# Kernel optimization log

Measured on AMD Instinct MI355X. Metric: run time of the kernel, lower is better.

## Reference

```python
import jax, jax.numpy as jnp
import numpy as np
from jax import lax


def _gru_pass(x_proj, h0, w_hh, b_hh):
    # Faithful to torch: unbatched GRU scanning sequentially over the n_sample axis
    # with a single shared hidden state. x_proj: (N, 3H) = x @ w_ih.T + b_ih.
    def cell(h, xp):
        gh = jnp.dot(w_hh, h) + b_hh              # (3H,)
        xr, xz, xn = jnp.split(xp, 3)
        hr, hz, hn = jnp.split(gh, 3)
        r = jax.nn.sigmoid(xr + hr)
        z = jax.nn.sigmoid(xz + hz)
        n = jnp.tanh(xn + r * hn)
        h_new = (1.0 - z) * n + z * h
        return h_new, h_new
    h_last, outs = lax.scan(cell, h0, x_proj)
    return outs, h_last                            # (N, H), (H,)


def setup_inputs() -> dict:
    key = jax.random.key(0)
    ks = jax.random.split(key, 6)
    H = 50
    s = 0.2  # ~ torch default init scale for these fan-ins
    return {
        "w_ih": jax.random.normal(ks[0], (3 * H, 2), jnp.float32) * s,
        "w_hh": jax.random.normal(ks[1], (3 * H, H), jnp.float32) * s,
        "b_ih": jax.random.normal(ks[2], (3 * H,), jnp.float32) * s,
        "b_hh": jax.random.normal(ks[3], (3 * H,), jnp.float32) * s,
        "fc_w": jax.random.normal(ks[4], (2, H), jnp.float32) * s,
        "fc_b": jax.random.normal(ks[5], (2,), jnp.float32) * s,
        "sorb": 64,
        "n_sample": 4096,
    }


def reference(w_ih, w_hh, b_ih, b_hh, fc_w, fc_b, sorb, n_sample):
    H = w_hh.shape[1]
    baseline = float(sorb // 2 - 1)
    base_key = jax.random.key(42)
    x0 = jnp.zeros((n_sample, 2), jnp.float32)     # samples[:, 0, :] == 0
    h0 = jnp.zeros((H,), jnp.float32)
    nup0 = jnp.zeros((n_sample,), jnp.float32)

    def heaviside(x):
        # 0.5*(sign(sign(x)+0.1)+1): 1 for x >= 0, else 0
        return (x >= 0.0).astype(jnp.float32)

    def step(carry, i):
        x, h, num_up = carry
        x_proj = x @ w_ih.T + b_ih                 # (N, 3H)
        outs, h_new = _gru_pass(x_proj, h, w_hh, b_hh)
        logits = outs @ fc_w.T + fc_b              # (N, 2)
        out = jnp.sqrt(jax.nn.softmax(logits, axis=1))  # sqsoftmax
        # occupation-number masking, active for i >= sorb/2
        num_down = i.astype(jnp.float32) - num_up
        act_up = heaviside(baseline - num_up)
        act_down = heaviside(baseline - num_down)
        masked = out * jnp.stack([act_down, act_up], axis=1)
        masked = masked / jnp.clip(
            jnp.linalg.norm(masked, axis=1, keepdims=True), 1e-30, None)
        out = jnp.where(i >= sorb / 2, masked, out)
        # multinomial over 2 classes (weights need not sum to 1)
        p0 = out[:, 0] / jnp.clip(out[:, 0] + out[:, 1], 1e-30, None)
        u = jax.random.uniform(jax.random.fold_in(base_key, i), (n_sample,))
        s = (u >= p0).astype(jnp.int32)            # 1 == class 1 ("up")
        x_next = jax.nn.one_hot(s, 2, dtype=jnp.float32)
        return (x_next, h_new, num_up + s.astype(jnp.float32)), s

    _, samples = lax.scan(step, (x0, h0, nup0), jnp.arange(sorb))
    # torch returns argmax over the one-hot == sampled class index
    return samples.T                                # (n_sample, sorb) int32
```

## Files before the change

### kernel.cpp

```cpp
#include <hip/hip_runtime.h>
#include <cstdint>

#pragma clang fp contract(off)

#define HH 50
#define SORB 64
#define NSAMP 4096
#define TOT (SORB * NSAMP)
#define RSLOTS 128
#define RSTRIDE 56
#define SPIN_FUEL (1 << 16)

typedef __attribute__((ext_vector_type(2))) float v2f;
typedef __attribute__((ext_vector_type(4))) float v4f;

__device__ __forceinline__ float xla_tanh(float x) {
  const float kClamp = 7.90531110763549805f;
  float ax = fabsf(x);
  float xc = fminf(fmaxf(x, -kClamp), kClamp);
  float x2 = xc * xc;
  float p = -2.76076847742355e-16f;
  p = x2 * p + 2.00018790482477e-13f;
  p = x2 * p + -8.60467152213735e-11f;
  p = x2 * p + 5.12229709037114e-08f;
  p = x2 * p + 1.48572235717979e-05f;
  p = x2 * p + 6.37261928875436e-04f;
  p = x2 * p + 4.89352455891786e-03f;
  p = xc * p;
  float q = 1.19825839466702e-06f;
  q = x2 * q + 1.18534705686654e-04f;
  q = x2 * q + 2.26843463243900e-03f;
  q = x2 * q + 4.89352518554385e-03f;
  float r = p / q;
  return (ax < 0.0004f) ? x : r;
}

__device__ __forceinline__ float xla_logistic(float x) {
  return 0.5f + 0.5f * xla_tanh(x * 0.5f);
}

__device__ __forceinline__ float exp_cr(float x) {
  return (float)exp((double)x);
}

__device__ __forceinline__ void tf2x32(uint32_t k0, uint32_t k1,
                                       uint32_t c0, uint32_t c1,
                                       uint32_t& o0, uint32_t& o1) {
  uint32_t k2 = k0 ^ k1 ^ 0x1BD11BDAu;
  uint32_t x0 = c0 + k0, x1 = c1 + k1;
#define TF_R(d) { x0 += x1; x1 = (x1 << (d)) | (x1 >> (32 - (d))); x1 ^= x0; }
#define TF_GA TF_R(13) TF_R(15) TF_R(26) TF_R(6)
#define TF_GB TF_R(17) TF_R(29) TF_R(16) TF_R(24)
  TF_GA; x0 += k1; x1 += k2 + 1u;
  TF_GB; x0 += k2; x1 += k0 + 2u;
  TF_GA; x0 += k0; x1 += k1 + 3u;
  TF_GB; x0 += k1; x1 += k2 + 4u;
  TF_GA; x0 += k2; x1 += k0 + 5u;
#undef TF_GB
#undef TF_GA
#undef TF_R
  o0 = x0; o1 = x1;
}

__device__ __forceinline__ float u_for_cell(int cc) {
  int ii = cc >> 12;
  int jj = cc & (NSAMP - 1);
  uint32_t k0, k1;
  tf2x32(0u, 42u, 0u, (uint32_t)ii, k0, k1);
  uint32_t b0, b1;
  tf2x32(k0, k1, 0u, (uint32_t)jj, b0, b1);
  uint32_t bits = b0 ^ b1;
  return __uint_as_float((bits >> 9) | 0x3f800000u) - 1.0f;
}

__device__ __forceinline__ float dot_xla(const v2f* __restrict__ w,
                                         const v2f* __restrict__ h) {
  v2f A0 = w[0] * h[0];
  v2f A1 = w[1] * h[1];
  v2f A2 = w[2] * h[2];
  v2f A3 = w[3] * h[3];
#pragma unroll
  for (int ch = 1; ch < 6; ++ch) {
    A0 = A0 + w[4 * ch + 0] * h[4 * ch + 0];
    A1 = A1 + w[4 * ch + 1] * h[4 * ch + 1];
    A2 = A2 + w[4 * ch + 2] * h[4 * ch + 2];
    A3 = A3 + w[4 * ch + 3] * h[4 * ch + 3];
  }
  v2f S0 = A0 + A2;
  v2f S1 = A1 + A3;
  v2f T = S0 + S1;
  float dot = T.x + T.y;
  dot = dot + w[24].x * h[24].x;
  dot = dot + w[24].y * h[24].y;
  return dot;
}

extern "C" __global__ void __launch_bounds__(128, 1)
ARSampler_59244778881183_kernel(const float* __restrict__ w_ih,
                                const float* __restrict__ w_hh,
                                const float* __restrict__ b_ih,
                                const float* __restrict__ b_hh,
                                const float* __restrict__ fc_w,
                                const float* __restrict__ fc_b,
                                int* __restrict__ out) {
  __shared__ __align__(16) float ring[RSLOTS][RSTRIDE];
  __shared__ float sh_nu[NSAMP];
  __shared__ unsigned char sh_bits[2][NSAMP];
  __shared__ unsigned int sh_done;

  const int t = threadIdx.x;
  const int lane = t & 63;

  if (t < 64) {
    for (int s = lane; s < RSLOTS; s += 64)
      ring[s][HH] = __uint_as_float(~0u);
    if (lane < HH) ring[RSLOTS - 1][lane] = 0.0f;
  } else {
    if (lane == 0) sh_done = 0u;
    for (int q = lane; q < NSAMP; q += 64) sh_nu[q] = 0.0f;
  }
  __syncthreads();

  if (t < 64) {
    const int tr = (lane < HH) ? lane : 0;

    v2f wA[25], wB[25], wC[25];
#pragma unroll
    for (int k = 0; k < 25; ++k) {
      wA[k] = v2f{w_hh[tr * HH + 2 * k], w_hh[tr * HH + 2 * k + 1]};
      wB[k] = v2f{w_hh[(tr + 50) * HH + 2 * k], w_hh[(tr + 50) * HH + 2 * k + 1]};
      wC[k] = v2f{w_hh[(tr + 100) * HH + 2 * k], w_hh[(tr + 100) * HH + 2 * k + 1]};
    }
    const float bhr = b_hh[tr], bhz = b_hh[tr + 50], bhn = b_hh[tr + 100];
    const float xrb = b_ih[tr], xzb = b_ih[tr + 50], xnb = b_ih[tr + 100];
    const float xr0 = w_ih[tr * 2 + 0] + xrb;
    const float xr1 = w_ih[tr * 2 + 1] + xrb;
    const float xz0 = w_ih[(tr + 50) * 2 + 0] + xzb;
    const float xz1 = w_ih[(tr + 50) * 2 + 1] + xzb;
    const float xn0 = w_ih[(tr + 100) * 2 + 0] + xnb;
    const float xn1 = w_ih[(tr + 100) * 2 + 1] + xnb;
    float hold = 0.0f;

    volatile unsigned int* donep = &sh_done;

    for (int c = 0; c < TOT; ++c) {
      const int i = c >> 12;
      const int j = c & (NSAMP - 1);

      if ((c & 63) == 0 && c >= RSLOTS) {
        int fuel = SPIN_FUEL;
        while (*donep < (unsigned)(c - 64) && --fuel)
          __builtin_amdgcn_s_sleep(2);
        asm volatile("" ::: "memory");
      }

      const float* rp = ring[(c + RSLOTS - 1) & (RSLOTS - 1)];
      v2f hv[25];
#pragma unroll
      for (int m = 0; m < 13; ++m) {
        v4f f = *(const v4f*)(rp + 4 * m);
        hv[2 * m] = v2f{f.x, f.y};
        if (2 * m + 1 < 25) hv[2 * m + 1] = v2f{f.z, f.w};
      }

      float xr, xz, xn;
      if (i == 0) {
        xr = xrb; xz = xzb; xn = xnb;
      } else {
        unsigned b = sh_bits[(i - 1) & 1][j];
        xr = b ? xr1 : xr0;
        xz = b ? xz1 : xz0;
        xn = b ? xn1 : xn0;
      }

      const float ghr = dot_xla(wA, hv) + bhr;
      const float ghz = dot_xla(wB, hv) + bhz;
      const float ghn = dot_xla(wC, hv) + bhn;

      const float r = xla_logistic(xr + ghr);
      const float z = xla_logistic(xz + ghz);
      const float rhn = r * ghn;
      const float n = xla_tanh(xn + rhn);
      const float omz = 1.0f - z;
      const float hnew = omz * n + z * hold;
      hold = hnew;

      const int wi = (lane < HH) ? lane : HH;
      const float wd = (lane < HH) ? hnew : __uint_as_float((unsigned)c);
      ring[c & (RSLOTS - 1)][wi] = wd;
    }
  } else {
    float fw0[HH], fw1[HH];
#pragma unroll
    for (int k = 0; k < HH; ++k) {
      fw0[k] = fc_w[k];
      fw1[k] = fc_w[HH + k];
    }
    const float fb0 = fc_b[0], fb1 = fc_b[1];

    for (int B = 0; B < TOT; B += 64) {
      const int cc = B + lane;
      const int ii = B >> 12;
      const int jj = cc & (NSAMP - 1);

      {
        const unsigned target = (unsigned)(B + 63);
        volatile unsigned int* sp =
            (volatile unsigned int*)&ring[(B + 63) & (RSLOTS - 1)][HH];
        int fuel = SPIN_FUEL;
        while (*sp != target && --fuel) __builtin_amdgcn_s_sleep(2);
        __builtin_amdgcn_s_sleep(1);
        asm volatile("s_waitcnt lgkmcnt(0)" ::: "memory");
      }

      const float* op = ring[cc & (RSLOTS - 1)];
      float o[52];
#pragma unroll
      for (int m = 0; m < 13; ++m) {
        v4f f = *(const v4f*)(op + 4 * m);
        o[4 * m + 0] = f.x; o[4 * m + 1] = f.y;
        o[4 * m + 2] = f.z; o[4 * m + 3] = f.w;
      }

      float l0 = 0.0f, l1 = 0.0f;
#pragma unroll
      for (int k = 0; k < HH; ++k) {
        l0 = fmaf(o[k], fw0[k], l0);
        l1 = fmaf(o[k], fw1[k], l1);
      }
      l0 = l0 + fb0;
      l1 = l1 + fb1;

      const float mx = fmaxf(l0, l1);
      const float e0 = exp_cr(l0 - mx);
      const float e1 = exp_cr(l1 - mx);
      const float se = e0 + e1;
      float o0 = sqrtf(e0 / se);
      float o1 = sqrtf(e1 / se);

      const float nuo = sh_nu[jj];
      if (ii >= SORB / 2) {
        const float fi = (float)ii;
        const float ndown = fi - nuo;
        const float ad = ((31.0f - ndown) >= 0.0f) ? 1.0f : 0.0f;
        const float au = ((31.0f - nuo) >= 0.0f) ? 1.0f : 0.0f;
        const float m0 = o0 * ad;
        const float m1 = o1 * au;
        float nr = sqrtf(m0 * m0 + m1 * m1);
        nr = fmaxf(nr, 1e-30f);
        o0 = m0 / nr;
        o1 = m1 / nr;
      }
      const float den = fmaxf(o0 + o1, 1e-30f);
      const float p0 = o0 / den;
      const float u = u_for_cell(cc);
      const int s = (u >= p0) ? 1 : 0;

      sh_nu[jj] = nuo + (float)s;
      sh_bits[ii & 1][jj] = (unsigned char)s;
      out[jj * SORB + ii] = s;

      asm volatile("" ::: "memory");
      *(volatile unsigned int*)&sh_done = (unsigned)(B + 64);
    }
  }
}

extern "C" void kernel_launch(void* const* d_in, const int* in_sizes, int n_in,
                              void* d_out, int out_size, void* d_ws, size_t ws_size,
                              hipStream_t stream) {
  (void)in_sizes; (void)n_in; (void)out_size; (void)d_ws; (void)ws_size;
  const float* w_ih = (const float*)d_in[0];
  const float* w_hh = (const float*)d_in[1];
  const float* b_ih = (const float*)d_in[2];
  const float* b_hh = (const float*)d_in[3];
  const float* fc_w = (const float*)d_in[4];
  const float* fc_b = (const float*)d_in[5];
  hipLaunchKernelGGL(ARSampler_59244778881183_kernel, dim3(1), dim3(128), 0, stream,
                     w_ih, w_hh, b_ih, b_hh, fc_w, fc_b, (int*)d_out);
}
```

Measured before the change: 169.6 ms.

## Split GRU gate matvecs across three wavefronts with LDS flag handoff

New measurement: 196.7 ms. 1.16x slower.

```diff
diff --git a/kernel.cpp b/kernel.cpp
--- a/kernel.cpp
+++ b/kernel.cpp
@@ -95,7 +95,14 @@
   return dot;
 }
 
-extern "C" __global__ void __launch_bounds__(128, 1)
+#define SPIN_EQ(addr, target) do {                                           \
+  volatile unsigned int* sp_ = (volatile unsigned int*)(addr);               \
+  int fuel_ = SPIN_FUEL;                                                     \
+  while (*sp_ != (unsigned)(target) && --fuel_) {}                           \
+  asm volatile("s_waitcnt lgkmcnt(0)" ::: "memory");                         \
+} while (0)
+
+extern "C" __global__ void __launch_bounds__(256, 1)
 ARSampler_59244778881183_kernel(const float* __restrict__ w_ih,
                                 const float* __restrict__ w_hh,
                                 const float* __restrict__ b_ih,
@@ -104,41 +111,40 @@
                                 const float* __restrict__ fc_b,
                                 int* __restrict__ out) {
   __shared__ __align__(16) float ring[RSLOTS][RSTRIDE];
+  __shared__ float ghr[RSTRIDE];
+  __shared__ float ghz[RSTRIDE];
   __shared__ float sh_nu[NSAMP];
   __shared__ unsigned char sh_bits[2][NSAMP];
   __shared__ unsigned int sh_done;
 
   const int t = threadIdx.x;
   const int lane = t & 63;
-
-  if (t < 64) {
+  const int wv = t >> 6;
+
+  if (wv == 0) {
     for (int s = lane; s < RSLOTS; s += 64)
       ring[s][HH] = __uint_as_float(~0u);
     if (lane < HH) ring[RSLOTS - 1][lane] = 0.0f;
-  } else {
+    if (lane == 0) ghr[HH] = __uint_as_float(~0u);
+    if (lane == 1) ghz[HH] = __uint_as_float(~0u);
+  } else if (wv == 3) {
     if (lane == 0) sh_done = 0u;
     for (int q = lane; q < NSAMP; q += 64) sh_nu[q] = 0.0f;
   }
   __syncthreads();
 
-  if (t < 64) {
+  if (wv < 3) {
     const int tr = (lane < HH) ? lane : 0;
-
-    v2f wA[25], wB[25], wC[25];
-#pragma unroll
-    for (int k = 0; k < 25; ++k) {
-      wA[k] = v2f{w_hh[tr * HH + 2 * k], w_hh[tr * HH + 2 * k + 1]};
-      wB[k] = v2f{w_hh[(tr + 50) * HH + 2 * k], w_hh[(tr + 50) * HH + 2 * k + 1]};
-      wC[k] = v2f{w_hh[(tr + 100) * HH + 2 * k], w_hh[(tr + 100) * HH + 2 * k + 1]};
-    }
-    const float bhr = b_hh[tr], bhz = b_hh[tr + 50], bhn = b_hh[tr + 100];
-    const float xrb = b_ih[tr], xzb = b_ih[tr + 50], xnb = b_ih[tr + 100];
-    const float xr0 = w_ih[tr * 2 + 0] + xrb;
-    const float xr1 = w_ih[tr * 2 + 1] + xrb;
-    const float xz0 = w_ih[(tr + 50) * 2 + 0] + xzb;
-    const float xz1 = w_ih[(tr + 50) * 2 + 1] + xzb;
-    const float xn0 = w_ih[(tr + 100) * 2 + 0] + xnb;
-    const float xn1 = w_ih[(tr + 100) * 2 + 1] + xnb;
+    const int row = tr + wv * 50;
+
+    v2f w[25];
+#pragma unroll
+    for (int k = 0; k < 25; ++k)
+      w[k] = v2f{w_hh[row * HH + 2 * k], w_hh[row * HH + 2 * k + 1]};
+    const float bh = b_hh[row];
+    const float xb = b_ih[row];
+    const float x0 = w_ih[row * 2 + 0] + xb;
+    const float x1 = w_ih[row * 2 + 1] + xb;
     float hold = 0.0f;
 
     volatile unsigned int* donep = &sh_done;
@@ -147,13 +153,14 @@
       const int i = c >> 12;
       const int j = c & (NSAMP - 1);
 
-      if ((c & 63) == 0 && c >= RSLOTS) {
+      if (wv == 2 && (c & 63) == 0 && c >= RSLOTS) {
         int fuel = SPIN_FUEL;
         while (*donep < (unsigned)(c - 64) && --fuel)
           __builtin_amdgcn_s_sleep(2);
         asm volatile("" ::: "memory");
       }
 
+      if (c > 0) SPIN_EQ(&ring[(c - 1) & (RSLOTS - 1)][HH], c - 1);
       const float* rp = ring[(c + RSLOTS - 1) & (RSLOTS - 1)];
       v2f hv[25];
 #pragma unroll
@@ -163,31 +170,40 @@
         if (2 * m + 1 < 25) hv[2 * m + 1] = v2f{f.z, f.w};
       }
 
-      float xr, xz, xn;
+      float xs;
       if (i == 0) {
-        xr = xrb; xz = xzb; xn = xnb;
+        xs = xb;
       } else {
         unsigned b = sh_bits[(i - 1) & 1][j];
-        xr = b ? xr1 : xr0;
-        xz = b ? xz1 : xz0;
-        xn = b ? xn1 : xn0;
-      }
-
-      const float ghr = dot_xla(wA, hv) + bhr;
-      const float ghz = dot_xla(wB, hv) + bhz;
-      const float ghn = dot_xla(wC, hv) + bhn;
-
-      const float r = xla_logistic(xr + ghr);
-      const float z = xla_logistic(xz + ghz);
-      const float rhn = r * ghn;
-      const float n = xla_tanh(xn + rhn);
-      const float omz = 1.0f - z;
-      const float hnew = omz * n + z * hold;
-      hold = hnew;
-
-      const int wi = (lane < HH) ? lane : HH;
-      const float wd = (lane < HH) ? hnew : __uint_as_float((unsigned)c);
-      ring[c & (RSLOTS - 1)][wi] = wd;
+        xs = b ? x1 : x0;
+      }
+
+      const float dot = dot_xla(w, hv);
+
+      if (wv == 0) {
+        const float vr = xs + (dot + bh);
+        ghr[(lane < HH) ? lane : (HH + 1)] = vr;
+        ghr[HH] = __uint_as_float((unsigned)c);
+      } else if (wv == 1) {
+        const float vz = xs + (dot + bh);
+        ghz[(lane < HH) ? lane : (HH + 1)] = vz;
+        ghz[HH] = __uint_as_float((unsigned)c);
+      } else {
+        const float ghn = dot + bh;
+        SPIN_EQ(&ghr[HH], c);
+        SPIN_EQ(&ghz[HH], c);
+        const float vr = ghr[tr];
+        const float vz = ghz[tr];
+        const float r = xla_logistic(vr);
+        const float z = xla_logistic(vz);
+        const float rhn = r * ghn;
+        const float n = xla_tanh(xs + rhn);
+        const float omz = 1.0f - z;
+        const float hnew = omz * n + z * hold;
+        hold = hnew;
+        ring[c & (RSLOTS - 1)][(lane < HH) ? lane : (HH + 1)] = hnew;
+        ring[c & (RSLOTS - 1)][HH] = __uint_as_float((unsigned)c);
+      }
     }
   } else {
     float fw0[HH], fw1[HH];
@@ -276,6 +292,6 @@
   const float* b_hh = (const float*)d_in[3];
   const float* fc_w = (const float*)d_in[4];
   const float* fc_b = (const float*)d_in[5];
-  hipLaunchKernelGGL(ARSampler_59244778881183_kernel, dim3(1), dim3(128), 0, stream,
+  hipLaunchKernelGGL(ARSampler_59244778881183_kernel, dim3(1), dim3(256), 0, stream,
                      w_ih, w_hh, b_ih, b_hh, fc_w, fc_b, (int*)d_out);
 }
```
